# Performance work log

Hardware: AMD Instinct MI355X
Metric: run time of the kernel (lower is better)

## Reference

```python
import jax, jax.numpy as jnp
import numpy as np

B, C, T = 4, 768, 512
H, KS, NL, W = 12, 3, 6, 4
D = C // H  # 64


def setup_inputs() -> dict:
    key = jax.random.key(0)
    ks = jax.random.split(key, 24)
    def n(k, shape, scale):
        return jax.random.normal(k, shape, dtype=jnp.float32) * scale
    cscale = C ** -0.5
    return {
        "x": jax.random.normal(ks[0], (B, C, T), dtype=jnp.float32),
        "x_mask": jnp.ones((B, 1, T), dtype=jnp.float32),
        "Wq": n(ks[1], (NL, C, C), cscale), "bq": jnp.zeros((NL, C), jnp.float32),
        "Wk": n(ks[2], (NL, C, C), cscale), "bk": jnp.zeros((NL, C), jnp.float32),
        "Wv": n(ks[3], (NL, C, C), cscale), "bv": jnp.zeros((NL, C), jnp.float32),
        "Wo": n(ks[4], (NL, C, C), cscale), "bo": jnp.zeros((NL, C), jnp.float32),
        "emb_rel_k": n(ks[5], (NL, D, 2 * W + 1), D ** -0.5),
        "emb_rel_v": n(ks[6], (NL, D, 2 * W + 1), D ** -0.5),
        "ffn_w1": n(ks[7], (NL, 4 * C, C, KS), (C * KS) ** -0.5),
        "ffn_b1": jnp.zeros((NL, 4 * C), jnp.float32),
        "ffn_w2": n(ks[8], (NL, C, 4 * C, KS), (4 * C * KS) ** -0.5),
        "ffn_b2": jnp.zeros((NL, C), jnp.float32),
        "norm1_g": jnp.ones((NL, C), jnp.float32), "norm1_b": jnp.zeros((NL, C), jnp.float32),
        "norm2_g": jnp.ones((NL, C), jnp.float32), "norm2_b": jnp.zeros((NL, C), jnp.float32),
    }


def _conv1x1(x, w, b):  # x:[B,C,T] w:[O,C] -> [B,O,T]
    return jnp.einsum('oc,bct->bot', w, x) + b[None, :, None]


def _conv1d(x, w, b, pad):  # x:[B,Ci,T] w:[O,Ci,K]
    y = jax.lax.conv_general_dilated(x, w, (1,), [(pad, pad)],
                                     dimension_numbers=('NCH', 'OIH', 'NCH'))
    return y + b[None, :, None]


def _layer_norm_c(x, g, b):  # normalize over channel dim of [B,C,T]
    m = jnp.mean(x, axis=1, keepdims=True)
    v = jnp.var(x, axis=1, keepdims=True)
    return (x - m) * jax.lax.rsqrt(v + 1e-5) * g[None, :, None] + b[None, :, None]


def _rel_to_abs(x):  # [b,h,l,2l-1] -> [b,h,l,l]
    b, h, l, _ = x.shape
    x = jnp.pad(x, ((0, 0), (0, 0), (0, 0), (0, 1)))
    x = x.reshape(b, h, l * 2 * l)
    x = jnp.pad(x, ((0, 0), (0, 0), (0, l - 1)))
    return x.reshape(b, h, l + 1, 2 * l - 1)[:, :, :l, l - 1:]


def _abs_to_rel(x):  # [b,h,l,l] -> [b,h,l,2l-1]
    b, h, l, _ = x.shape
    x = jnp.pad(x, ((0, 0), (0, 0), (0, 0), (0, l - 1)))
    x = x.reshape(b, h, l * l + l * (l - 1))
    x = jnp.pad(x, ((0, 0), (0, 0), (l, 0)))
    return x.reshape(b, h, l, 2 * l)[:, :, :, 1:]


def _get_rel_emb(emb, t, w):  # emb:[D,2w+1] -> [D,2t-1]
    pad = max(t - (w + 1), 0)
    start = max(w + 1 - t, 0)
    e = jnp.pad(emb, ((0, 0), (pad, pad)))
    return e[:, start:start + 2 * t - 1]


def _attention(x, attn_mask, wq, bq, wk, bk, wv, bv, wo, bo, ek, ev):
    b, c, t = x.shape
    scale = D ** 0.5
    q = _conv1x1(x, wq, bq).reshape(b, H, D, t)
    k = _conv1x1(x, wk, bk).reshape(b, H, D, t)
    v = _conv1x1(x, wv, bv).reshape(b, H, D, t)
    scores = jnp.einsum('bhdt,bhds->bhts', q, k) / scale  # [b,H,t,t]
    k_emb = _get_rel_emb(ek, t, W)  # [D,2t-1]
    rel_logits = jnp.einsum('bhdt,dr->bhtr', q / scale, k_emb)
    scores = scores + _rel_to_abs(rel_logits)
    scores = jnp.where(attn_mask == 0, -10000.0, scores)
    p = jax.nn.softmax(scores, axis=-1)
    out = jnp.einsum('bhts,bhds->bhdt', p, v)
    v_emb = _get_rel_emb(ev, t, W)  # [D,2t-1]
    out = out + jnp.einsum('bhtr,dr->bhdt', _abs_to_rel(p), v_emb)
    return _conv1x1(out.reshape(b, c, t), wo, bo)


def _ffn(x, x_mask, w1, b1, w2, b2):
    y = _conv1d(x * x_mask, w1, b1, KS // 2)
    y = jax.nn.gelu(y, approximate=False)
    y = _conv1d(y * x_mask, w2, b2, KS // 2)
    return y * x_mask


def reference(x, x_mask, Wq, bq, Wk, bk, Wv, bv, Wo, bo, emb_rel_k, emb_rel_v,
              ffn_w1, ffn_b1, ffn_w2, ffn_b2, norm1_g, norm1_b, norm2_g, norm2_b):
    attn_mask = x_mask[:, :, None, :] * x_mask[:, :, :, None]  # [B,1,T,T]
    for i in range(NL):
        y = _attention(x, attn_mask, Wq[i], bq[i], Wk[i], bk[i], Wv[i], bv[i],
                       Wo[i], bo[i], emb_rel_k[i], emb_rel_v[i])
        x = _layer_norm_c(x + y, norm1_g[i], norm1_b[i])
        y = _ffn(x, x_mask, ffn_w1[i], ffn_b1[i], ffn_w2[i], ffn_b2[i])
        x = _layer_norm_c(x + y, norm2_g[i], norm2_b[i])
        x = x * x_mask
    return x
```

## Files before the change

### kernel.cpp

```cpp
#include <hip/hip_runtime.h>
#include <cstddef>

namespace {

constexpr int B  = 4;
constexpr int C  = 768;
constexpr int T  = 512;
constexpr int H  = 12;
constexpr int D  = 64;
constexpr int NL = 6;
constexpr int W  = 4;
constexpr int FF = 3072;

typedef __attribute__((ext_vector_type(8))) short sh8;
typedef __attribute__((ext_vector_type(4))) float f32x4;

__device__ inline float gelu_exact(float x) {
  return 0.5f * x * (1.0f + erff(x * 0.70710678118654752440f));
}
__device__ inline unsigned short f2b(float f) {
  unsigned u = __float_as_uint(f);
  unsigned r = (u + 0x7fffu + ((u >> 16) & 1u)) >> 16;
  return (unsigned short)r;
}
__device__ inline float b2f(unsigned short u) {
  return __uint_as_float((unsigned)u << 16);
}
__device__ inline void gload_lds16(const void* g, void* l) {
  __builtin_amdgcn_global_load_lds(
      (const __attribute__((address_space(1))) unsigned int*)g,
      (__attribute__((address_space(3))) unsigned int*)l, 16, 0, 0);
}

__global__ __launch_bounds__(256) void transpose_cvt_in(
    const float* __restrict__ s, unsigned short* __restrict__ dh,
    float* __restrict__ df)
{
  __shared__ float tile[32][33];
  const int b = blockIdx.z;
  const int c0 = blockIdx.y * 32, t0 = blockIdx.x * 32;
  const int tx = threadIdx.x & 31, ty = threadIdx.x >> 5;
  const float* sp = s + ((size_t)b * C + c0) * T + t0;
#pragma unroll
  for (int i = 0; i < 4; ++i)
    tile[ty + i * 8][tx] = sp[(size_t)(ty + i * 8) * T + tx];
  __syncthreads();
  unsigned short* dph = dh + ((size_t)b * T + t0) * C + c0;
  float* dpf = df + ((size_t)b * T + t0) * C + c0;
#pragma unroll
  for (int i = 0; i < 4; ++i) {
    const float v = tile[tx][ty + i * 8];
    dph[(size_t)(ty + i * 8) * C + tx] = f2b(v);
    dpf[(size_t)(ty + i * 8) * C + tx] = v;
  }
}

__global__ __launch_bounds__(256) void transpose_out(
    const float* __restrict__ s, float* __restrict__ d)
{
  __shared__ float tile[32][33];
  const int b = blockIdx.z;
  const int c0 = blockIdx.y * 32, t0 = blockIdx.x * 32;
  const int tx = threadIdx.x & 31, ty = threadIdx.x >> 5;
  const float* sp = s + ((size_t)b * T + t0) * C + c0;
#pragma unroll
  for (int i = 0; i < 4; ++i)
    tile[ty + i * 8][tx] = sp[(size_t)(ty + i * 8) * C + tx];
  __syncthreads();
  float* dp = d + ((size_t)b * C + c0) * T + t0;
#pragma unroll
  for (int i = 0; i < 4; ++i)
    dp[(size_t)(ty + i * 8) * T + tx] = tile[tx][ty + i * 8];
}

__global__ __launch_bounds__(256) void cvt_qkvo_tiled(
    const float* __restrict__ q, const float* __restrict__ k,
    const float* __restrict__ v, const float* __restrict__ o,
    unsigned short* __restrict__ dq, unsigned short* __restrict__ dk,
    unsigned short* __restrict__ dv, unsigned short* __restrict__ dov)
{
  __shared__ float lds[16][132];
  const int z = blockIdx.y;
  const size_t loff = (size_t)blockIdx.z * C * C;
  const float* s = (z == 0 ? q : z == 1 ? k : z == 2 ? v : o) + loff;
  unsigned short* d = (z == 0 ? dq : z == 1 ? dk : z == 2 ? dv : dov) + loff;
  constexpr int KST = C / 32;
  constexpr int KSG = KST / 4;
  const int mt = blockIdx.x / KSG;
  const int ksg = blockIdx.x % KSG;
  const int tid = threadIdx.x;
#pragma unroll
  for (int p = 0; p < 2; ++p) {
    const int f = tid + p * 256;
    const int row = f >> 5, c4 = f & 31;
    float4 vv = *(const float4*)(s + (size_t)(mt * 16 + row) * C + ksg * 128 + c4 * 4);
    *(float4*)&lds[row][c4 * 4] = vv;
  }
  __syncthreads();
  const int ksl = tid >> 6, lane = tid & 63;
  const int l15 = lane & 15, lhi = lane >> 4;
  float4 a = *(const float4*)&lds[l15][ksl * 32 + lhi * 8];
  float4 b = *(const float4*)&lds[l15][ksl * 32 + lhi * 8 + 4];
  sh8 u;
  u[0] = (short)f2b(a.x); u[1] = (short)f2b(a.y);
  u[2] = (short)f2b(a.z); u[3] = (short)f2b(a.w);
  u[4] = (short)f2b(b.x); u[5] = (short)f2b(b.y);
  u[6] = (short)f2b(b.z); u[7] = (short)f2b(b.w);
  *(sh8*)(d + ((size_t)(mt * KST + ksg * 4 + ksl) * 64 + lane) * 8) = u;
}

__global__ __launch_bounds__(256) void cvt_ffn_tiled(
    const float* __restrict__ s1, const float* __restrict__ s2,
    unsigned short* __restrict__ d1, unsigned short* __restrict__ d2)
{
  __shared__ float lds[16][388];
  const int z = blockIdx.y;
  const int layer = blockIdx.z;
  const float* src = (z ? s2 : s1) + (size_t)layer * FF * C * 3;
  unsigned short* dst = (z ? d2 : d1) + (size_t)layer * 3 * FF * C;
  const int O  = z ? C : FF;
  const int Ci = z ? FF : C;
  const int KST = Ci >> 5;
  const int KSG = KST >> 2;
  const int mt = blockIdx.x / KSG;
  const int ksg = blockIdx.x % KSG;
  const int tid = threadIdx.x;
  const size_t rowlen = (size_t)Ci * 3;
#pragma unroll
  for (int p = 0; p < 6; ++p) {
    const int f = tid + p * 256;
    const int row = f / 96, c4 = f % 96;
    float4 vv = *(const float4*)(src + (size_t)(mt * 16 + row) * rowlen +
                                 ksg * 384 + c4 * 4);
    *(float4*)&lds[row][c4 * 4] = vv;
  }
  __syncthreads();
  const int ksl = tid >> 6, lane = tid & 63;
  const int l15 = lane & 15, lhi = lane >> 4;
  const int q0 = ksl * 96 + lhi * 24;
  float f[24];
#pragma unroll
  for (int kq = 0; kq < 6; ++kq) {
    float4 t4 = *(const float4*)&lds[l15][q0 + kq * 4];
    f[kq * 4 + 0] = t4.x; f[kq * 4 + 1] = t4.y;
    f[kq * 4 + 2] = t4.z; f[kq * 4 + 3] = t4.w;
  }
  const size_t fragoff = ((size_t)(mt * KST + ksg * 4 + ksl) * 64 + lane) * 8;
#pragma unroll
  for (int tap = 0; tap < 3; ++tap) {
    sh8 u;
#pragma unroll
    for (int j = 0; j < 8; ++j) u[j] = (short)f2b(f[j * 3 + tap]);
    *(sh8*)(dst + (size_t)tap * O * Ci + fragoff) = u;
  }
}

template <int TAPS, int BN, int KSPLIT, bool GELU, bool MASK_OUT, bool OBF16>
__global__ __launch_bounds__(256) void mfma_conv(
    const unsigned short* __restrict__ xin,
    const unsigned short* __restrict__ w0p, const unsigned short* __restrict__ w1p,
    const unsigned short* __restrict__ w2p,
    const float* __restrict__ b0, const float* __restrict__ b1,
    const float* __restrict__ b2,
    const float* __restrict__ mask,
    void* __restrict__ o0p, void* __restrict__ o1p, void* __restrict__ o2p,
    int Cin, int O, int tilesPerPlane, int nz)
{
  constexpr int ROWS_B = BN + TAPS - 1;
  constexpr int PB = 40;
  constexpr int NPASS = BN / 64;
  constexpr int NF = BN / 32;
  constexpr int NT = T / BN;
  __shared__ unsigned short Aw[2][TAPS * 8 * 512];
  __shared__ unsigned short Bx[2][ROWS_B * PB];

  const int nwg = gridDim.x;
  const int orig = blockIdx.x;
  const int wg = (orig & 7) * (nwg >> 3) + (orig >> 3);
  const int txt = wg % NT;
  const int rest = wg / NT;
  const int zz = rest % nz;
  const int ty = rest / nz;

  const int b  = zz / KSPLIT;
  const int kk = zz % KSPLIT;
  const int TOFF = (TAPS == 3) ? -1 : 0;
  const int t0 = txt * BN;
  const int plane = ty / tilesPerPlane;
  const int mt0 = (ty % tilesPerPlane) * 8;
  const int o0 = mt0 * 16;

  const int tid = threadIdx.x;
  const int lane = tid & 63, wid = tid >> 6;
  const int wm = wid >> 1, wn = wid & 1;
  const int l15 = lane & 15, lhi = lane >> 4;
  const int bmask = b * T;

  const unsigned short* wsel = plane == 0 ? w0p : (plane == 1 ? w1p : w2p);
  const float* bp = plane == 0 ? b0 : (plane == 1 ? b1 : b2);

  const int KST = Cin >> 5;
  const int kchunk = KST / KSPLIT;
  const int ks0 = kk * kchunk, ks1 = ks0 + kchunk;
  const int OT = O >> 4;

  const unsigned short* xb_ = xin + (size_t)b * T * Cin;

  sh8 breg[NPASS], breg2;
  auto stageA = [&](int ks, int buf) {
#pragma unroll
    for (int tap = 0; tap < TAPS; ++tap) {
#pragma unroll
      for (int j = 0; j < 2; ++j) {
        const int rt = wid * 2 + j;
        const unsigned short* src =
            wsel + (((size_t)tap * OT + mt0 + rt) * KST + ks) * 512 + lane * 8;
        gload_lds16(src, &Aw[buf][(tap * 8 + rt) * 512]);
      }
    }
  };
  auto loadB = [&](int ks) {
    const int c0 = ks << 5;
#pragma unroll
    for (int p = 0; p < NPASS; ++p) {
      const int idx = tid + p * 256;
      const int row = idx >> 2, c8 = (idx & 3) << 3;
      const int tsrc = t0 + row + TOFF;
      breg[p] = (sh8)0;
      if ((unsigned)tsrc < (unsigned)T)
        breg[p] = *(const sh8*)(xb_ + (size_t)tsrc * Cin + c0 + c8);
    }
    if constexpr (TAPS == 3) {
      breg2 = (sh8)0;
      if (tid < 8) {
        const int row = BN + (tid >> 2), c8 = (tid & 3) << 3;
        const int ts2 = t0 + row + TOFF;
        if ((unsigned)ts2 < (unsigned)T)
          breg2 = *(const sh8*)(xb_ + (size_t)ts2 * Cin + c0 + c8);
      }
    }
  };
  auto writeB = [&](int buf) {
#pragma unroll
    for (int p = 0; p < NPASS; ++p) {
      const int idx = tid + p * 256;
      *(sh8*)&Bx[buf][(idx >> 2) * PB + ((idx & 3) << 3)] = breg[p];
    }
    if constexpr (TAPS == 3) {
      if (tid < 8)
        *(sh8*)&Bx[buf][(BN + (tid >> 2)) * PB + ((tid & 3) << 3)] = breg2;
    }
  };

  f32x4 acc[4][NF] = {};

  int cur = 0;
  stageA(ks0, 0);
  loadB(ks0);
  writeB(0);
  __syncthreads();

  for (int ks = ks0; ks < ks1; ++ks) {
    const int nxt = cur ^ 1;
    const bool more = (ks + 1 < ks1);
    if (more) { stageA(ks + 1, nxt); loadB(ks + 1); }
#pragma unroll
    for (int tap = 0; tap < TAPS; ++tap) {
      sh8 af[4], bfr[NF];
#pragma unroll
      for (int m = 0; m < 4; ++m)
        af[m] = *(const sh8*)&Aw[cur][(tap * 8 + wm * 4 + m) * 512 + lane * 8];
#pragma unroll
      for (int n = 0; n < NF; ++n)
        bfr[n] = *(const sh8*)&Bx[cur][(wn * (NF * 16) + n * 16 + l15 + tap) * PB + lhi * 8];
#pragma unroll
      for (int m = 0; m < 4; ++m)
#pragma unroll
        for (int n = 0; n < NF; ++n)
          acc[m][n] = __builtin_amdgcn_mfma_f32_16x16x32_bf16(
              af[m], bfr[n], acc[m][n], 0, 0, 0);
    }
    if (more) writeB(nxt);
    __syncthreads();
    cur = nxt;
  }

  void* obase = plane == 0 ? o0p : (plane == 1 ? o1p : o2p);
  unsigned short* oph = (unsigned short*)obase + (size_t)b * T * O;
  float* opf = (float*)obase + ((size_t)kk * B + b) * (size_t)T * O;
#pragma unroll
  for (int m = 0; m < 4; ++m) {
    const int o = o0 + (wm * 4 + m) * 16 + (lhi << 2);
#pragma unroll
    for (int n = 0; n < NF; ++n) {
      const int t = t0 + wn * (NF * 16) + n * 16 + l15;
      const float mk = MASK_OUT ? mask[bmask + t] : 1.f;
      float v[4];
#pragma unroll
      for (int r4 = 0; r4 < 4; ++r4) {
        float x = acc[m][n][r4];
        if (KSPLIT > 1) {
          if (kk == 0) x += bp[o + r4];
        } else {
          x += bp[o + r4];
        }
        if (GELU) x = gelu_exact(x);
        if (MASK_OUT) x *= mk;
        v[r4] = x;
      }
      if constexpr (OBF16) {
        ushort4 hz;
        hz.x = f2b(v[0]); hz.y = f2b(v[1]); hz.z = f2b(v[2]); hz.w = f2b(v[3]);
        *(ushort4*)(oph + (size_t)t * O + o) = hz;
      } else {
        *(float4*)(opf + (size_t)t * O + o) = make_float4(v[0], v[1], v[2], v[3]);
      }
    }
  }
}

__global__ __launch_bounds__(256) void fused_attn(
    const unsigned short* __restrict__ qg,
    const unsigned short* __restrict__ kg,
    const unsigned short* __restrict__ vg,
    const float* __restrict__ mask,
    const float* __restrict__ ek,
    const float* __restrict__ ev,
    unsigned short* __restrict__ outp)
{
  constexpr int PITCH = 72;
  __shared__ unsigned short Qs[64 * PITCH];
  __shared__ unsigned short Ks[2][64 * PITCH];
  __shared__ unsigned short Vs[2][64 * PITCH];
  __shared__ unsigned short Ps[64 * PITCH];
  __shared__ float eks[D * 9], evs[D * 9];
  __shared__ float qekl[64 * 12];
  __shared__ float mks[2][64];

  const int t0 = blockIdx.x * 64;
  const int bh = blockIdx.y;
  const int b = bh / H, h = bh % H;
  const int tid = threadIdx.x;
  const int lane = tid & 63, w = tid >> 6;
  const int l15 = lane & 15, lhi = lane >> 4;

  const size_t base = (size_t)b * T * C + h * D;
  const unsigned short* qh = qg + base;
  const unsigned short* kh = kg + base;
  const unsigned short* vh = vg + base;

  for (int e = tid; e < D * 9; e += 256) { eks[e] = ek[e]; evs[e] = ev[e]; }
  {
    const int tl = tid & 63, d0 = (tid >> 6) << 4;
    const unsigned short* src = qh + (size_t)(t0 + tl) * C + d0;
    *(sh8*)&Qs[tl * PITCH + d0]     = *(const sh8*)(src);
    *(sh8*)&Qs[tl * PITCH + d0 + 8] = *(const sh8*)(src + 8);
  }
  __syncthreads();
  {
    const int tl = tid & 63, g = tid >> 6;
    for (int j = g; j < 9; j += 4) {
      float a = 0.f;
      for (int d = 0; d < D; ++d)
        a = fmaf(b2f(Qs[tl * PITCH + d]), eks[d * 9 + j], a);
      qekl[tl * 12 + j] = a * 0.125f;
    }
  }
  const int t_loc = w * 16 + l15;
  const int t = t0 + t_loc;
  const float mask_t = mask[b * T + t];
  const sh8 bq0 = *(const sh8*)&Qs[t_loc * PITCH + lhi * 8];
  const sh8 bq1 = *(const sh8*)&Qs[t_loc * PITCH + 32 + lhi * 8];

  const int sl = tid & 63, d0s = (tid >> 6) << 4;
  {
    const unsigned short* srck = kh + (size_t)sl * C + d0s;
    *(sh8*)&Ks[0][sl * PITCH + d0s]     = *(const sh8*)(srck);
    *(sh8*)&Ks[0][sl * PITCH + d0s + 8] = *(const sh8*)(srck + 8);
    const unsigned short* srcv = vh + (size_t)sl * C + d0s;
    sh8 u0 = *(const sh8*)(srcv);
    sh8 u1 = *(const sh8*)(srcv + 8);
#pragma unroll
    for (int j = 0; j < 8; ++j) Vs[0][(d0s + j) * PITCH + sl] = (unsigned short)u0[j];
#pragma unroll
    for (int j = 0; j < 8; ++j) Vs[0][(d0s + 8 + j) * PITCH + sl] = (unsigned short)u1[j];
    if (tid < 64) mks[0][tid] = mask[b * T + tid];
  }
  __syncthreads();

  float m_run = -1e30f, l_run = 0.f;
  f32x4 oacc[4] = {};
  int cur = 0;
  sh8 kr0, kr1, vr0, vr1;
  float mkr = 0.f;

  for (int s0 = 0; s0 < T; s0 += 64) {
    const int nxt = cur ^ 1;
    const bool more = (s0 + 64 < T);
    if (more) {
      const unsigned short* srck = kh + (size_t)(s0 + 64 + sl) * C + d0s;
      kr0 = *(const sh8*)(srck);
      kr1 = *(const sh8*)(srck + 8);
      const unsigned short* srcv = vh + (size_t)(s0 + 64 + sl) * C + d0s;
      vr0 = *(const sh8*)(srcv);
      vr1 = *(const sh8*)(srcv + 8);
      if (tid < 64) mkr = mask[b * T + s0 + 64 + tid];
    }

    float p[16];
#pragma unroll
    for (int n = 0; n < 4; ++n) {
      const sh8 a0 = *(const sh8*)&Ks[cur][(n * 16 + l15) * PITCH + lhi * 8];
      const sh8 a1 = *(const sh8*)&Ks[cur][(n * 16 + l15) * PITCH + 32 + lhi * 8];
      f32x4 acc = {};
      acc = __builtin_amdgcn_mfma_f32_16x16x32_bf16(a0, bq0, acc, 0, 0, 0);
      acc = __builtin_amdgcn_mfma_f32_16x16x32_bf16(a1, bq1, acc, 0, 0, 0);
#pragma unroll
      for (int r = 0; r < 4; ++r) {
        const int s = s0 + n * 16 + lhi * 4 + r;
        float v = acc[r] * 0.125f;
        const int j = s - t + 4;
        if ((unsigned)j < 9u) v += qekl[t_loc * 12 + j];
        if (mask_t * mks[cur][s - s0] == 0.f) v = -10000.0f;
        p[n * 4 + r] = v;
      }
    }
    float mloc = p[0];
#pragma unroll
    for (int i = 1; i < 16; ++i) mloc = fmaxf(mloc, p[i]);
    mloc = fmaxf(mloc, __shfl_xor(mloc, 16));
    mloc = fmaxf(mloc, __shfl_xor(mloc, 32));
    const float m_new = fmaxf(m_run, mloc);
    const float f = __expf(m_run - m_new);
    float sloc = 0.f;
#pragma unroll
    for (int i = 0; i < 16; ++i) { p[i] = __expf(p[i] - m_new); sloc += p[i]; }
    sloc += __shfl_xor(sloc, 16);
    sloc += __shfl_xor(sloc, 32);
    l_run = l_run * f + sloc;
    m_run = m_new;
#pragma unroll
    for (int m = 0; m < 4; ++m)
#pragma unroll
      for (int r = 0; r < 4; ++r) oacc[m][r] *= f;
#pragma unroll
    for (int n = 0; n < 4; ++n) {
      uint2 pk;
      pk.x = (unsigned)f2b(p[n * 4 + 0]) | ((unsigned)f2b(p[n * 4 + 1]) << 16);
      pk.y = (unsigned)f2b(p[n * 4 + 2]) | ((unsigned)f2b(p[n * 4 + 3]) << 16);
      *(uint2*)&Ps[t_loc * PITCH + n * 16 + lhi * 4] = pk;
    }
    asm volatile("s_waitcnt lgkmcnt(0)" ::: "memory");
    const sh8 bp0 = *(const sh8*)&Ps[t_loc * PITCH + lhi * 8];
    const sh8 bp1 = *(const sh8*)&Ps[t_loc * PITCH + 32 + lhi * 8];
#pragma unroll
    for (int m = 0; m < 4; ++m) {
      const sh8 a0 = *(const sh8*)&Vs[cur][(m * 16 + l15) * PITCH + lhi * 8];
      const sh8 a1 = *(const sh8*)&Vs[cur][(m * 16 + l15) * PITCH + 32 + lhi * 8];
      oacc[m] = __builtin_amdgcn_mfma_f32_16x16x32_bf16(a0, bp0, oacc[m], 0, 0, 0);
      oacc[m] = __builtin_amdgcn_mfma_f32_16x16x32_bf16(a1, bp1, oacc[m], 0, 0, 0);
    }
    if (t + 4 >= s0 && t < s0 + 68) {
#pragma unroll
      for (int j = 0; j < 9; ++j) {
        const int s = t + j - 4;
        if (s >= s0 && s < s0 + 64) {
          const float pv = b2f(Ps[t_loc * PITCH + (s - s0)]);
#pragma unroll
          for (int m = 0; m < 4; ++m)
#pragma unroll
            for (int r = 0; r < 4; ++r)
              oacc[m][r] = fmaf(pv, evs[(m * 16 + lhi * 4 + r) * 9 + j], oacc[m][r]);
        }
      }
    }
    if (more) {
      *(sh8*)&Ks[nxt][sl * PITCH + d0s]     = kr0;
      *(sh8*)&Ks[nxt][sl * PITCH + d0s + 8] = kr1;
#pragma unroll
      for (int j = 0; j < 8; ++j) Vs[nxt][(d0s + j) * PITCH + sl] = (unsigned short)vr0[j];
#pragma unroll
      for (int j = 0; j < 8; ++j) Vs[nxt][(d0s + 8 + j) * PITCH + sl] = (unsigned short)vr1[j];
      if (tid < 64) mks[nxt][tid] = mkr;
    }
    __syncthreads();
    cur = nxt;
  }
  const float invl = 1.f / l_run;
  unsigned short* ob = outp + (size_t)(b * T + t) * C + h * D;
#pragma unroll
  for (int m = 0; m < 4; ++m) {
    ushort4 hz;
    hz.x = f2b(oacc[m][0] * invl);
    hz.y = f2b(oacc[m][1] * invl);
    hz.z = f2b(oacc[m][2] * invl);
    hz.w = f2b(oacc[m][3] * invl);
    *(ushort4*)(ob + m * 16 + lhi * 4) = hz;
  }
}

template <int NP, bool MASKY, bool MASKF>
__global__ __launch_bounds__(256) void add_norm_wave(
    const float* __restrict__ xr, const float* __restrict__ ypart,
    const float* __restrict__ g, const float* __restrict__ bta,
    const float* __restrict__ mask, float* __restrict__ dst,
    unsigned short* __restrict__ dsth)
{
  const int b = blockIdx.y;
  const int t = blockIdx.x * 4 + (threadIdx.x >> 6);
  const int lane = threadIdx.x & 63;
  const float mkt = mask[b * T + t];
  const size_t rowoff = ((size_t)b * T + t) * C;
  const int ci0 = lane * 12;

  float vv[12];
  float sum = 0.f, sq = 0.f;
#pragma unroll
  for (int q = 0; q < 3; ++q) {
    const int ci = ci0 + q * 4;
    float4 xv = *(const float4*)(xr + rowoff + ci);
    float4 yv = make_float4(0.f, 0.f, 0.f, 0.f);
#pragma unroll
    for (int p = 0; p < NP; ++p) {
      float4 t4 = *(const float4*)(ypart + (size_t)p * B * T * C + rowoff + ci);
      yv.x += t4.x; yv.y += t4.y; yv.z += t4.z; yv.w += t4.w;
    }
    if (MASKY) { yv.x *= mkt; yv.y *= mkt; yv.z *= mkt; yv.w *= mkt; }
    const float v0 = xv.x + yv.x, v1 = xv.y + yv.y;
    const float v2 = xv.z + yv.z, v3 = xv.w + yv.w;
    vv[q * 4 + 0] = v0; vv[q * 4 + 1] = v1; vv[q * 4 + 2] = v2; vv[q * 4 + 3] = v3;
    sum += v0 + v1 + v2 + v3;
    sq = fmaf(v0, v0, fmaf(v1, v1, fmaf(v2, v2, fmaf(v3, v3, sq))));
  }
#pragma unroll
  for (int o = 32; o > 0; o >>= 1) {
    sum += __shfl_xor(sum, o);
    sq += __shfl_xor(sq, o);
  }
  const float m = sum * (1.f / C);
  const float rs = rsqrtf(sq * (1.f / C) - m * m + 1e-5f);
#pragma unroll
  for (int q = 0; q < 3; ++q) {
    const int ci = ci0 + q * 4;
    float4 gv = *(const float4*)(g + ci);
    float4 bv = *(const float4*)(bta + ci);
    float o0 = (vv[q * 4 + 0] - m) * rs * gv.x + bv.x;
    float o1 = (vv[q * 4 + 1] - m) * rs * gv.y + bv.y;
    float o2 = (vv[q * 4 + 2] - m) * rs * gv.z + bv.z;
    float o3 = (vv[q * 4 + 3] - m) * rs * gv.w + bv.w;
    if (MASKF) { o0 *= mkt; o1 *= mkt; o2 *= mkt; o3 *= mkt; }
    *(float4*)(dst + rowoff + ci) = make_float4(o0, o1, o2, o3);
    const float hm = MASKF ? 1.f : mkt;
    ushort4 hz;
    hz.x = f2b(o0 * hm); hz.y = f2b(o1 * hm); hz.z = f2b(o2 * hm); hz.w = f2b(o3 * hm);
    *(ushort4*)(dsth + rowoff + ci) = hz;
  }
}

}

extern "C" void kernel_launch(void* const* d_in, const int* in_sizes, int n_in,
                              void* d_out, int out_size, void* d_ws, size_t ws_size,
                              hipStream_t stream) {
  const float* x_in = (const float*)d_in[0];
  const float* mask = (const float*)d_in[1];
  const float* Wq = (const float*)d_in[2];
  const float* bq = (const float*)d_in[3];
  const float* Wk = (const float*)d_in[4];
  const float* bk = (const float*)d_in[5];
  const float* Wv = (const float*)d_in[6];
  const float* bv = (const float*)d_in[7];
  const float* Wo = (const float*)d_in[8];
  const float* bo = (const float*)d_in[9];
  const float* ek = (const float*)d_in[10];
  const float* ev = (const float*)d_in[11];
  const float* w1 = (const float*)d_in[12];
  const float* b1 = (const float*)d_in[13];
  const float* w2 = (const float*)d_in[14];
  const float* b2 = (const float*)d_in[15];
  const float* n1g = (const float*)d_in[16];
  const float* n1b = (const float*)d_in[17];
  const float* n2g = (const float*)d_in[18];
  const float* n2b = (const float*)d_in[19];

  float* ws = (float*)d_ws;
  const size_t SZ_X = (size_t)B * C * T;
  const size_t SZ_W1 = (size_t)3 * FF * C;
  float* xr    = ws;
  float* xr1   = xr + SZ_X;
  float* ypart = xr1 + SZ_X;
  unsigned short* xbh = (unsigned short*)(ypart + 4 * SZ_X);
  unsigned short* xfh = xbh + SZ_X;
  unsigned short* qbh = xfh + SZ_X;
  unsigned short* kbh = qbh + SZ_X;
  unsigned short* vbh = kbh + SZ_X;
  unsigned short* hidh = vbh + SZ_X;
  unsigned short* w1t = hidh + (size_t)B * FF * T;
  unsigned short* w2t = w1t + (size_t)NL * SZ_W1;
  unsigned short* wqt = w2t + (size_t)NL * SZ_W1;
  unsigned short* wkt = wqt + (size_t)NL * C * C;
  unsigned short* wvt = wkt + (size_t)NL * C * C;
  unsigned short* wot = wvt + (size_t)NL * C * C;
  float* outp = (float*)d_out;

  const dim3 blk(256);
  transpose_cvt_in<<<dim3(T / 32, C / 32, B), blk, 0, stream>>>(x_in, xbh, xr);
  cvt_qkvo_tiled<<<dim3((C / 16) * (C / 128), 4, NL), blk, 0, stream>>>(
      Wq, Wk, Wv, Wo, wqt, wkt, wvt, wot);
  cvt_ffn_tiled<<<dim3((FF / 16) * (C / 128), 2, NL), blk, 0, stream>>>(
      w1, w2, w1t, w2t);

  for (int i = 0; i < NL; ++i) {
    const size_t wOff = (size_t)i * C * C;
    const unsigned short* w1l = w1t + (size_t)i * SZ_W1;
    const unsigned short* w2l = w2t + (size_t)i * SZ_W1;
    mfma_conv<1, 64, 1, false, false, true><<<dim3(8 * 18 * 4), blk, 0, stream>>>(
        xbh, wqt + wOff, wkt + wOff, wvt + wOff,
        bq + i * C, bk + i * C, bv + i * C, mask,
        qbh, kbh, vbh, C, C, 6, 4);
    fused_attn<<<dim3(T / 64, B * H), blk, 0, stream>>>(
        qbh, kbh, vbh, mask, ek + (size_t)i * D * 9, ev + (size_t)i * D * 9, hidh);
    mfma_conv<1, 64, 3, false, false, false><<<dim3(8 * 6 * 12), blk, 0, stream>>>(
        hidh, wot + wOff, wot + wOff, wot + wOff,
        bo + i * C, bo + i * C, bo + i * C, mask,
        ypart, ypart, ypart, C, C, 6, 12);
    add_norm_wave<3, false, false><<<dim3(T / 4, B), blk, 0, stream>>>(
        xr, ypart, n1g + i * C, n1b + i * C, mask, xr1, xfh);
    mfma_conv<3, 128, 1, true, true, true><<<dim3(4 * 24 * 4), blk, 0, stream>>>(
        xfh, w1l, w1l, w1l, b1 + i * FF, b1 + i * FF, b1 + i * FF, mask,
        hidh, hidh, hidh, C, FF, 24, 4);
    mfma_conv<3, 128, 4, false, false, false><<<dim3(4 * 6 * 16), blk, 0, stream>>>(
        hidh, w2l, w2l, w2l, b2 + i * C, b2 + i * C, b2 + i * C, mask,
        ypart, ypart, ypart, FF, C, 6, 16);
    add_norm_wave<4, true, true><<<dim3(T / 4, B), blk, 0, stream>>>(
        xr1, ypart, n2g + i * C, n2b + i * C, mask, xr, xbh);
  }
  transpose_out<<<dim3(T / 32, C / 32, B), blk, 0, stream>>>(xr, outp);
}
```

Before: 1.182 ms.

## Store attention and FFN hidden activations in K-blocked layout; add setprio and nontemporal loads

Changes the intermediate activation layout written by fused_attn and the FFN1 conv to a channel-blocked [B][C/32][T][32] format, and has the consuming convs read B tiles from it. Each 32-channel k-step then reads contiguous 64-byte rows instead of rows strided by the full channel count, which is meant to improve coalescing. It also raises wave priority around MFMA sequences in attention and uses nontemporal loads in the weight conversion kernels. Producers and consumers must agree on the layout, which adds template complexity.

```diff
diff --git a/kernel.cpp b/kernel.cpp
--- a/kernel.cpp
+++ b/kernel.cpp
@@ -93,8 +93,9 @@
   for (int p = 0; p < 2; ++p) {
     const int f = tid + p * 256;
     const int row = f >> 5, c4 = f & 31;
-    float4 vv = *(const float4*)(s + (size_t)(mt * 16 + row) * C + ksg * 128 + c4 * 4);
-    *(float4*)&lds[row][c4 * 4] = vv;
+    f32x4 vv = __builtin_nontemporal_load(
+        (const f32x4*)(s + (size_t)(mt * 16 + row) * C + ksg * 128 + c4 * 4));
+    *(f32x4*)&lds[row][c4 * 4] = vv;
   }
   __syncthreads();
   const int ksl = tid >> 6, lane = tid & 63;
@@ -130,9 +131,9 @@
   for (int p = 0; p < 6; ++p) {
     const int f = tid + p * 256;
     const int row = f / 96, c4 = f % 96;
-    float4 vv = *(const float4*)(src + (size_t)(mt * 16 + row) * rowlen +
-                                 ksg * 384 + c4 * 4);
-    *(float4*)&lds[row][c4 * 4] = vv;
+    f32x4 vv = __builtin_nontemporal_load(
+        (const f32x4*)(src + (size_t)(mt * 16 + row) * rowlen + ksg * 384 + c4 * 4));
+    *(f32x4*)&lds[row][c4 * 4] = vv;
   }
   __syncthreads();
   const int ksl = tid >> 6, lane = tid & 63;
@@ -155,7 +156,8 @@
   }
 }
 
-template <int TAPS, int BN, int KSPLIT, bool GELU, bool MASK_OUT, bool OBF16>
+template <int TAPS, int BN, int KSPLIT, bool GELU, bool MASK_OUT, bool OBF16,
+          bool KBIN, bool KBOUT>
 __global__ __launch_bounds__(256) void mfma_conv(
     const unsigned short* __restrict__ xin,
     const unsigned short* __restrict__ w0p, const unsigned short* __restrict__ w1p,
@@ -205,6 +207,7 @@
   const int OT = O >> 4;
 
   const unsigned short* xb_ = xin + (size_t)b * T * Cin;
+  const unsigned short* xkb = xin + (size_t)b * KST * T * 32;
 
   sh8 breg[NPASS], breg2;
   auto stageA = [&](int ks, int buf) {
@@ -221,22 +224,31 @@
   };
   auto loadB = [&](int ks) {
     const int c0 = ks << 5;
+    const unsigned short* kbase = xkb + (size_t)ks * T * 32;
 #pragma unroll
     for (int p = 0; p < NPASS; ++p) {
       const int idx = tid + p * 256;
       const int row = idx >> 2, c8 = (idx & 3) << 3;
       const int tsrc = t0 + row + TOFF;
       breg[p] = (sh8)0;
-      if ((unsigned)tsrc < (unsigned)T)
-        breg[p] = *(const sh8*)(xb_ + (size_t)tsrc * Cin + c0 + c8);
+      if ((unsigned)tsrc < (unsigned)T) {
+        if constexpr (KBIN)
+          breg[p] = *(const sh8*)(kbase + (size_t)tsrc * 32 + c8);
+        else
+          breg[p] = *(const sh8*)(xb_ + (size_t)tsrc * Cin + c0 + c8);
+      }
     }
     if constexpr (TAPS == 3) {
       breg2 = (sh8)0;
       if (tid < 8) {
         const int row = BN + (tid >> 2), c8 = (tid & 3) << 3;
         const int ts2 = t0 + row + TOFF;
-        if ((unsigned)ts2 < (unsigned)T)
-          breg2 = *(const sh8*)(xb_ + (size_t)ts2 * Cin + c0 + c8);
+        if ((unsigned)ts2 < (unsigned)T) {
+          if constexpr (KBIN)
+            breg2 = *(const sh8*)(kbase + (size_t)ts2 * 32 + c8);
+          else
+            breg2 = *(const sh8*)(xb_ + (size_t)ts2 * Cin + c0 + c8);
+        }
       }
     }
   };
@@ -287,6 +299,7 @@
 
   void* obase = plane == 0 ? o0p : (plane == 1 ? o1p : o2p);
   unsigned short* oph = (unsigned short*)obase + (size_t)b * T * O;
+  unsigned short* opk = (unsigned short*)obase + (size_t)b * (O >> 5) * T * 32;
   float* opf = (float*)obase + ((size_t)kk * B + b) * (size_t)T * O;
 #pragma unroll
   for (int m = 0; m < 4; ++m) {
@@ -311,7 +324,10 @@
       if constexpr (OBF16) {
         ushort4 hz;
         hz.x = f2b(v[0]); hz.y = f2b(v[1]); hz.z = f2b(v[2]); hz.w = f2b(v[3]);
-        *(ushort4*)(oph + (size_t)t * O + o) = hz;
+        if constexpr (KBOUT)
+          *(ushort4*)(opk + ((size_t)(o >> 5) * T + t) * 32 + (o & 31)) = hz;
+        else
+          *(ushort4*)(oph + (size_t)t * O + o) = hz;
       } else {
         *(float4*)(opf + (size_t)t * O + o) = make_float4(v[0], v[1], v[2], v[3]);
       }
@@ -413,8 +429,10 @@
       const sh8 a0 = *(const sh8*)&Ks[cur][(n * 16 + l15) * PITCH + lhi * 8];
       const sh8 a1 = *(const sh8*)&Ks[cur][(n * 16 + l15) * PITCH + 32 + lhi * 8];
       f32x4 acc = {};
+      __builtin_amdgcn_s_setprio(1);
       acc = __builtin_amdgcn_mfma_f32_16x16x32_bf16(a0, bq0, acc, 0, 0, 0);
       acc = __builtin_amdgcn_mfma_f32_16x16x32_bf16(a1, bq1, acc, 0, 0, 0);
+      __builtin_amdgcn_s_setprio(0);
 #pragma unroll
       for (int r = 0; r < 4; ++r) {
         const int s = s0 + n * 16 + lhi * 4 + r;
@@ -453,6 +471,7 @@
     asm volatile("s_waitcnt lgkmcnt(0)" ::: "memory");
     const sh8 bp0 = *(const sh8*)&Ps[t_loc * PITCH + lhi * 8];
     const sh8 bp1 = *(const sh8*)&Ps[t_loc * PITCH + 32 + lhi * 8];
+    __builtin_amdgcn_s_setprio(1);
 #pragma unroll
     for (int m = 0; m < 4; ++m) {
       const sh8 a0 = *(const sh8*)&Vs[cur][(m * 16 + l15) * PITCH + lhi * 8];
@@ -460,6 +479,7 @@
       oacc[m] = __builtin_amdgcn_mfma_f32_16x16x32_bf16(a0, bp0, oacc[m], 0, 0, 0);
       oacc[m] = __builtin_amdgcn_mfma_f32_16x16x32_bf16(a1, bp1, oacc[m], 0, 0, 0);
     }
+    __builtin_amdgcn_s_setprio(0);
     if (t + 4 >= s0 && t < s0 + 68) {
 #pragma unroll
       for (int j = 0; j < 9; ++j) {
@@ -487,7 +507,7 @@
     cur = nxt;
   }
   const float invl = 1.f / l_run;
-  unsigned short* ob = outp + (size_t)(b * T + t) * C + h * D;
+  unsigned short* okb = outp + (size_t)b * (C >> 5) * T * 32;
 #pragma unroll
   for (int m = 0; m < 4; ++m) {
     ushort4 hz;
@@ -495,7 +515,8 @@
     hz.y = f2b(oacc[m][1] * invl);
     hz.z = f2b(oacc[m][2] * invl);
     hz.w = f2b(oacc[m][3] * invl);
-    *(ushort4*)(ob + m * 16 + lhi * 4) = hz;
+    const int c = h * D + m * 16 + lhi * 4;
+    *(ushort4*)(okb + ((size_t)(c >> 5) * T + t) * 32 + (c & 31)) = hz;
   }
 }
 
@@ -614,22 +635,26 @@
     const size_t wOff = (size_t)i * C * C;
     const unsigned short* w1l = w1t + (size_t)i * SZ_W1;
     const unsigned short* w2l = w2t + (size_t)i * SZ_W1;
-    mfma_conv<1, 64, 1, false, false, true><<<dim3(8 * 18 * 4), blk, 0, stream>>>(
+    mfma_conv<1, 64, 1, false, false, true, false, false>
+        <<<dim3(8 * 18 * 4), blk, 0, stream>>>(
         xbh, wqt + wOff, wkt + wOff, wvt + wOff,
         bq + i * C, bk + i * C, bv + i * C, mask,
         qbh, kbh, vbh, C, C, 6, 4);
     fused_attn<<<dim3(T / 64, B * H), blk, 0, stream>>>(
         qbh, kbh, vbh, mask, ek + (size_t)i * D * 9, ev + (size_t)i * D * 9, hidh);
-    mfma_conv<1, 64, 3, false, false, false><<<dim3(8 * 6 * 12), blk, 0, stream>>>(
+    mfma_conv<1, 64, 3, false, false, false, true, false>
+        <<<dim3(8 * 6 * 12), blk, 0, stream>>>(
         hidh, wot + wOff, wot + wOff, wot + wOff,
         bo + i * C, bo + i * C, bo + i * C, mask,
         ypart, ypart, ypart, C, C, 6, 12);
     add_norm_wave<3, false, false><<<dim3(T / 4, B), blk, 0, stream>>>(
         xr, ypart, n1g + i * C, n1b + i * C, mask, xr1, xfh);
-    mfma_conv<3, 128, 1, true, true, true><<<dim3(4 * 24 * 4), blk, 0, stream>>>(
+    mfma_conv<3, 128, 1, true, true, true, false, true>
+        <<<dim3(4 * 24 * 4), blk, 0, stream>>>(
         xfh, w1l, w1l, w1l, b1 + i * FF, b1 + i * FF, b1 + i * FF, mask,
         hidh, hidh, hidh, C, FF, 24, 4);
-    mfma_conv<3, 128, 4, false, false, false><<<dim3(4 * 6 * 16), blk, 0, stream>>>(
+    mfma_conv<3, 128, 4, false, false, false, true, false>
+        <<<dim3(4 * 6 * 16), blk, 0, stream>>>(
         hidh, w2l, w2l, w2l, b2 + i * C, b2 + i * C, b2 + i * C, mask,
         ypart, ypart, ypart, FF, C, 6, 16);
     add_norm_wave<4, true, true><<<dim3(T / 4, B), blk, 0, stream>>>(
```

Result: faster. 1.104 ms, median of 2 (-6.6%).
